# Performance work log

Hardware: AMD Instinct MI355X
Metric: run time of the kernel (lower is better)

The kernel has to match this reference:

```python
import math
import jax, jax.numpy as jnp
import numpy as np

B, D, COND, H, K, L, BOUND = 262144, 16, 8, 128, 10, 4, 1.0
D2 = math.ceil(D / 2)          # second split (spline-transformed channels) = 8
D1 = D - D2                    # passthrough channels = 8
DOUT = (3 * K + 1) * D2        # subnet output = 248
PMIN = 1e-3                    # BIN_WIDTH_MIN == BIN_HEIGHT_MIN == DELTA_MIN


def setup_inputs() -> dict:
    key = jax.random.key(0)
    ks = jax.random.split(key, 8)
    x = jax.random.normal(ks[0], (B, D), dtype=jnp.float32)
    c = jax.random.normal(ks[1], (B, COND), dtype=jnp.float32)
    din1 = D1 + COND
    W1s = jax.random.normal(ks[2], (L, din1, H), dtype=jnp.float32) * 0.1
    b1s = jnp.zeros((L, H), dtype=jnp.float32)
    Whs = jax.random.normal(ks[3], (L, H, H), dtype=jnp.float32) * 0.1
    bhs = jnp.zeros((L, H), dtype=jnp.float32)
    Wos = jax.random.normal(ks[4], (L, H, DOUT), dtype=jnp.float32) * 0.1
    bos = jnp.zeros((L, DOUT), dtype=jnp.float32)
    rng = np.random.default_rng(0)  # permutation_seed = 0
    perms = jnp.asarray(np.stack([rng.permutation(D) for _ in range(L)]), dtype=jnp.int32)
    return {"x": x, "c": c, "W1s": W1s, "b1s": b1s, "Whs": Whs, "bhs": bhs,
            "Wos": Wos, "bos": bos, "perms": perms}


def _softmax_with_min(t, m):
    return m + (1.0 - m * t.shape[-1]) * jax.nn.softmax(t, axis=-1)


def _unpack_theta(theta):
    # theta: [B, D2, 3K+1]
    bw_u, bh_u, ks_u = theta[..., :K], theta[..., K:2 * K], theta[..., 2 * K:]
    bin_w = 2.0 * BOUND * _softmax_with_min(bw_u, PMIN)
    bin_h = 2.0 * BOUND * _softmax_with_min(bh_u, PMIN)
    slopes = PMIN + (1.0 - PMIN) * jax.nn.softplus(ks_u) / math.log(2.0)
    pad = ((0, 0), (0, 0), (1, 0))
    x_knots = jnp.pad(jnp.cumsum(bin_w, axis=-1), pad) - BOUND
    y_knots = jnp.pad(jnp.cumsum(bin_h, axis=-1), pad) - BOUND
    return x_knots, y_knots, bin_w, bin_h, slopes


def _spline_fwd(x2, x_knots, y_knots, bin_w, bin_h, slopes):
    # x2: [B, D2]; knots: [B, D2, K+1]; widths/heights: [B, D2, K]; slopes: [B, D2, K+1]
    bin_idx = jnp.sum(x_knots < x2[..., None], axis=-1) - 1  # searchsorted(left) - 1
    in_bounds = (bin_idx >= 0) & (bin_idx < K)
    ci = jnp.clip(bin_idx, 0, K - 1)
    g = lambda t, i: jnp.take_along_axis(t, i[..., None], axis=-1)[..., 0]
    x1, y1 = g(x_knots, ci), g(y_knots, ci)
    xw, yw = g(bin_w, ci), g(bin_h, ci)
    d1, d2 = g(slopes, ci), g(slopes, ci + 1)
    # safe x so rational-quadratic never produces nan for masked-out lanes
    xs = jnp.where(in_bounds, x2, x1 + 0.5 * xw)
    s = yw / xw
    eta = (xs - x1) / xw
    rev_eta = 1.0 - eta
    err = eta * rev_eta
    y_denom = s + (d1 + d2 - 2.0 * s) * err
    y_rq = y1 + yw * (s * eta ** 2 + d1 * err) / y_denom
    jac_num = s ** 2 * (d2 * eta ** 2 + 2.0 * s * err + d1 * rev_eta ** 2)
    log_jac = jnp.log(jac_num) - 2.0 * jnp.log(y_denom)
    # out-of-bounds: linear extrapolation through the outermost knots
    xl, xr = x_knots[..., 0], x_knots[..., -1]
    yb, yt = y_knots[..., 0], y_knots[..., -1]
    y_lin = (yt - yb) / (xr - xl) * (x2 - xl) + yb
    yx = jnp.where(in_bounds, y_rq, y_lin)
    log_jac = jnp.where(in_bounds, log_jac, 0.0)
    return yx, jnp.sum(log_jac, axis=-1)


def _flow_forward(x, c, W1s, b1s, Whs, bhs, Wos, bos, perms):
    log_jac_det = jnp.zeros((x.shape[0],), dtype=x.dtype)
    for i in range(L):
        x1, x2 = x[:, :D1], x[:, D1:]
        h = jax.nn.relu(jnp.concatenate([x1, c], axis=1) @ W1s[i] + b1s[i])
        h = jax.nn.relu(h @ Whs[i] + bhs[i])
        theta = (h @ Wos[i] + bos[i]).reshape(-1, D2, 3 * K + 1)
        x_knots, y_knots, bin_w, bin_h, slopes = _unpack_theta(theta)
        y2, ljd = _spline_fwd(x2, x_knots, y_knots, bin_w, bin_h, slopes)
        log_jac_det = log_jac_det + ljd
        x_out = jnp.concatenate([x1, y2], axis=1)
        x = jnp.take(x_out, perms[i], axis=1)  # x @ channel_perm.T
    return x, log_jac_det


def reference(x, c, W1s, b1s, Whs, bhs, Wos, bos, perms):
    return _flow_forward(x, c, W1s, b1s, Whs, bhs, Wos, bos, perms)
```

## Files before the change

kernel.cpp:

```cpp
#include <hip/hip_runtime.h>

#define B_N   262144
#define PMIN_F 0.001f
#define LOG2E 1.44269504088896340736f
#define LN2   0.69314718055994530942f

typedef _Float16 half4v __attribute__((ext_vector_type(4)));
typedef _Float16 half8  __attribute__((ext_vector_type(8)));
typedef float    floatx4 __attribute__((ext_vector_type(4)));

__device__ __forceinline__ float fexp2(float x) { return __builtin_amdgcn_exp2f(x); }
__device__ __forceinline__ float flog2(float x) { return __builtin_amdgcn_logf(x); }
__device__ __forceinline__ float frcp (float x) { return __builtin_amdgcn_rcpf(x); }

#define SB() __builtin_amdgcn_sched_barrier(0)

__global__ __launch_bounds__(64) void prep_kernel(
    const float* __restrict__ W1s, const float* __restrict__ b1s,
    const float* __restrict__ Whs, const float* __restrict__ Wos,
    _Float16* __restrict__ ws)
{
    const int bid   = blockIdx.x;
    const int layer = bid / 104;
    const int r     = bid % 104;
    const int lane  = threadIdx.x;
    const int kg    = lane >> 4;
    const int c     = lane & 15;

    half8 v;
    if (r < 8) {
        const int nt = r, n = nt * 16 + c;
        const float* W1 = W1s + layer * 16 * 128;
        const float* b1 = b1s + layer * 128;
        #pragma unroll
        for (int j = 0; j < 8; ++j) {
            const int k = kg * 8 + j;
            v[j] = (k < 16) ? (_Float16)W1[k * 128 + n]
                 : (k == 16) ? (_Float16)b1[n] : (_Float16)0.f;
        }
    } else if (r < 40) {
        const int f = r - 8, nt = f >> 2, ks = f & 3, n = nt * 16 + c;
        const float* Wh = Whs + layer * 128 * 128;
        #pragma unroll
        for (int j = 0; j < 8; ++j) {
            const int k = ks * 32 + kg * 8 + j;
            v[j] = (_Float16)Wh[k * 128 + n];
        }
    } else {
        const int f = r - 40, nt = f >> 2, ks = f & 3, n = nt * 16 + c;
        const int dd = n >> 5, cc = n & 31;
        const float* Wo = Wos + layer * 128 * 248;
        #pragma unroll
        for (int j = 0; j < 8; ++j) {
            const int k = ks * 32 + kg * 8 + j;
            v[j] = (cc < 31) ? (_Float16)Wo[k * 248 + dd * 31 + cc] : (_Float16)0.f;
        }
    }
    *(half8*)(ws + (size_t)bid * 512 + lane * 8) = v;
}

__device__ __forceinline__ void spline_eval(const float* __restrict__ Rf, const int base,
                                            const float x2, float& yout, float& ljout)
{
    const float4 v0 = *(const float4*)&Rf[base];
    const float4 v1 = *(const float4*)&Rf[base + 4];
    const float4 v2 = *(const float4*)&Rf[base + 8];
    const float4 v3 = *(const float4*)&Rf[base + 12];
    const float4 v4 = *(const float4*)&Rf[base + 16];

    float tw[10] = {v0.x, v0.y, v0.z, v0.w, v1.x, v1.y, v1.z, v1.w, v2.x, v2.y};
    float m1 = tw[0];
    #pragma unroll
    for (int i = 1; i < 10; ++i) m1 = fmaxf(m1, tw[i]);
    float se = 0.f;
    #pragma unroll
    for (int i = 0; i < 10; ++i) { tw[i] = fexp2((tw[i] - m1) * LOG2E); se += tw[i]; }
    const float inv198 = 1.98f * frcp(se);

    int cnt = 0;
    {
        float run = -1.f;
        cnt += (run < x2) ? 1 : 0;
        #pragma unroll
        for (int i = 0; i < 10; ++i) {
            run = run + fmaf(tw[i], inv198, 0.002f);
            cnt += (run < x2) ? 1 : 0;
        }
    }
    const int bidx = cnt - 1;
    const bool inb = (bidx >= 0) && (bidx < 10);
    const int ci = bidx < 0 ? 0 : (bidx > 9 ? 9 : bidx);

    float xlo = -1.f, xhi = 0.f, rx;
    {
        float run = -1.f;
        #pragma unroll
        for (int i = 0; i < 10; ++i) {
            const bool pick = (i == ci);
            xlo = pick ? run : xlo;
            run = run + fmaf(tw[i], inv198, 0.002f);
            xhi = pick ? run : xhi;
        }
        rx = run;
    }

    float hh[10] = {v2.z, v2.w, v3.x, v3.y, v3.z, v3.w, v4.x, v4.y, v4.z, v4.w};
    float hm = hh[0];
    #pragma unroll
    for (int i = 1; i < 10; ++i) hm = fmaxf(hm, hh[i]);
    float seh = 0.f;
    #pragma unroll
    for (int i = 0; i < 10; ++i) { hh[i] = fexp2((hh[i] - hm) * LOG2E); seh += hh[i]; }
    const float invh = 1.98f * frcp(seh);
    float ylo = -1.f, yhi = 0.f, ry;
    {
        float run = -1.f;
        #pragma unroll
        for (int i = 0; i < 10; ++i) {
            const bool pick = (i == ci);
            ylo = pick ? run : ylo;
            run = run + fmaf(hh[i], invh, 0.002f);
            yhi = pick ? run : yhi;
        }
        ry = run;
    }

    const float xw = xhi - xlo, yw = yhi - ylo;

    const float u1 = Rf[base + 20 + ci];
    const float u2 = Rf[base + 21 + ci];
    const float t1 = u1 * LOG2E;
    const float t2s = u2 * LOG2E;
    const float dd1 = PMIN_F + 0.999f * ((t1  > 15.f) ? t1  : flog2(1.f + fexp2(t1)));
    const float dd2 = PMIN_F + 0.999f * ((t2s > 15.f) ? t2s : flog2(1.f + fexp2(t2s)));

    const float xs  = inb ? x2 : (xlo + 0.5f * xw);
    const float rxw = frcp(xw);
    const float s   = yw * rxw;
    const float eta = (xs - xlo) * rxw;
    const float rev = 1.f - eta;
    const float er  = eta * rev;
    const float dn  = s + (dd1 + dd2 - 2.f * s) * er;
    const float yrq = ylo + yw * (s * eta * eta + dd1 * er) * frcp(dn);
    const float jn  = s * s * (dd2 * eta * eta + 2.f * s * er + dd1 * rev * rev);
    const float ljx = LN2 * (flog2(jn) - 2.f * flog2(dn));
    const float ylin = (ry + 1.f) * frcp(rx + 1.f) * (x2 + 1.f) - 1.f;

    yout  = inb ? yrq : ylin;
    ljout = inb ? ljx : 0.f;
}

__global__ __launch_bounds__(64, 3) void flow_mfma(
    const float* __restrict__ x_in,
    const float* __restrict__ c_in,
    const float* __restrict__ bhs,
    const float* __restrict__ bos,
    const int*   __restrict__ perms,
    const _Float16* __restrict__ wsW,
    float* __restrict__ out)
{
    __shared__ __align__(16) float    xls[2][256];
    __shared__ __align__(16) _Float16 R[2][2176];

    const int lane = threadIdx.x;
    const int q    = lane >> 4;
    const int m    = lane & 15;
    const long long row0 = (long long)blockIdx.x * 32;

    {
        const float4* xp = (const float4*)(x_in + row0 * 16);
        *(float4*)&xls[0][lane * 4] = xp[lane];
        *(float4*)&xls[1][lane * 4] = xp[lane + 64];
    }

    half8 a1c[2];
    #pragma unroll
    for (int t2 = 0; t2 < 2; ++t2) {
        #pragma unroll
        for (int j = 0; j < 8; ++j) a1c[t2][j] = (_Float16)0.f;
        if (q == 1) {
            const float4* cp = (const float4*)(c_in + (row0 + t2 * 16 + m) * 8);
            const float4 c0 = cp[0], c1 = cp[1];
            a1c[t2][0] = (_Float16)c0.x; a1c[t2][1] = (_Float16)c0.y;
            a1c[t2][2] = (_Float16)c0.z; a1c[t2][3] = (_Float16)c0.w;
            a1c[t2][4] = (_Float16)c1.x; a1c[t2][5] = (_Float16)c1.y;
            a1c[t2][6] = (_Float16)c1.z; a1c[t2][7] = (_Float16)c1.w;
        } else if (q == 2) {
            a1c[t2][0] = (_Float16)1.f;
        }
    }

    const int sp_t2  = lane >> 5;
    const int sp_row = (lane & 31) >> 1;
    const int sp_dl  = lane & 1;

    float ljacc = 0.f;

    for (int l = 0; l < 4; ++l) {
        const _Float16* wsl = wsW + (size_t)l * 104 * 512;
        const float* bh = bhs + l * 128;
        const float* bo = bos + l * 248;

        half8 bf1[8];
        #pragma unroll
        for (int i = 0; i < 8; ++i)
            bf1[i] = *(const half8*)(wsl + i * 512 + lane * 8);
        SB();

        half8 a1[2];
        #pragma unroll
        for (int t2 = 0; t2 < 2; ++t2) {
            a1[t2] = a1c[t2];
            if (q == 0) {
                const float4 lo = *(const float4*)&xls[t2][m * 16];
                const float4 hi = *(const float4*)&xls[t2][m * 16 + 4];
                a1[t2][0] = (_Float16)lo.x; a1[t2][1] = (_Float16)lo.y;
                a1[t2][2] = (_Float16)lo.z; a1[t2][3] = (_Float16)lo.w;
                a1[t2][4] = (_Float16)hi.x; a1[t2][5] = (_Float16)hi.y;
                a1[t2][6] = (_Float16)hi.z; a1[t2][7] = (_Float16)hi.w;
            }
        }
        #pragma unroll
        for (int g = 0; g < 2; ++g) {
            const floatx4 z = {0.f, 0.f, 0.f, 0.f};
            floatx4 acc0[4], acc1[4];
            #pragma unroll
            for (int nt = 0; nt < 4; ++nt) {
                acc0[nt] = __builtin_amdgcn_mfma_f32_16x16x32_f16(a1[0], bf1[g * 4 + nt], z, 0, 0, 0);
                acc1[nt] = __builtin_amdgcn_mfma_f32_16x16x32_f16(a1[1], bf1[g * 4 + nt], z, 0, 0, 0);
            }
            #pragma unroll
            for (int nt = 0; nt < 4; ++nt)
                #pragma unroll
                for (int reg = 0; reg < 4; ++reg) {
                    R[0][(q * 4 + reg) * 132 + (g * 4 + nt) * 16 + m] = (_Float16)fmaxf(acc0[nt][reg], 0.f);
                    R[1][(q * 4 + reg) * 132 + (g * 4 + nt) * 16 + m] = (_Float16)fmaxf(acc1[nt][reg], 0.f);
                }
        }

        half8 bf2a[16];
        #pragma unroll
        for (int i = 0; i < 16; ++i)
            bf2a[i] = *(const half8*)(wsl + (8 + i) * 512 + lane * 8);
        SB();

        half8 a2[2][4];
        #pragma unroll
        for (int t2 = 0; t2 < 2; ++t2)
            #pragma unroll
            for (int ks = 0; ks < 4; ++ks) {
                const half4v lo = *(const half4v*)&R[t2][m * 132 + ks * 32 + q * 8];
                const half4v hi = *(const half4v*)&R[t2][m * 132 + ks * 32 + q * 8 + 4];
                a2[t2][ks] = __builtin_shufflevector(lo, hi, 0, 1, 2, 3, 4, 5, 6, 7);
            }

        floatx4 accA0[4], accA1[4];
        #pragma unroll
        for (int nt = 0; nt < 4; ++nt) {
            const float bb = bh[nt * 16 + m];
            accA0[nt][0] = bb; accA0[nt][1] = bb; accA0[nt][2] = bb; accA0[nt][3] = bb;
            accA1[nt] = accA0[nt];
        }
        #pragma unroll
        for (int ks = 0; ks < 4; ++ks)
            #pragma unroll
            for (int nt = 0; nt < 4; ++nt) {
                accA0[nt] = __builtin_amdgcn_mfma_f32_16x16x32_f16(a2[0][ks], bf2a[nt * 4 + ks], accA0[nt], 0, 0, 0);
                accA1[nt] = __builtin_amdgcn_mfma_f32_16x16x32_f16(a2[1][ks], bf2a[nt * 4 + ks], accA1[nt], 0, 0, 0);
            }

        half8 bf2b[16];
        #pragma unroll
        for (int i = 0; i < 16; ++i)
            bf2b[i] = *(const half8*)(wsl + (24 + i) * 512 + lane * 8);
        SB();

        #pragma unroll
        for (int nt = 0; nt < 4; ++nt)
            #pragma unroll
            for (int reg = 0; reg < 4; ++reg) {
                R[0][(q * 4 + reg) * 132 + nt * 16 + m] = (_Float16)fmaxf(accA0[nt][reg], 0.f);
                R[1][(q * 4 + reg) * 132 + nt * 16 + m] = (_Float16)fmaxf(accA1[nt][reg], 0.f);
            }

        floatx4 accB0[4], accB1[4];
        #pragma unroll
        for (int nt = 0; nt < 4; ++nt) {
            const float bb = bh[(4 + nt) * 16 + m];
            accB0[nt][0] = bb; accB0[nt][1] = bb; accB0[nt][2] = bb; accB0[nt][3] = bb;
            accB1[nt] = accB0[nt];
        }
        #pragma unroll
        for (int ks = 0; ks < 4; ++ks)
            #pragma unroll
            for (int nt = 0; nt < 4; ++nt) {
                accB0[nt] = __builtin_amdgcn_mfma_f32_16x16x32_f16(a2[0][ks], bf2b[nt * 4 + ks], accB0[nt], 0, 0, 0);
                accB1[nt] = __builtin_amdgcn_mfma_f32_16x16x32_f16(a2[1][ks], bf2b[nt * 4 + ks], accB1[nt], 0, 0, 0);
            }
        #pragma unroll
        for (int nt = 0; nt < 4; ++nt)
            #pragma unroll
            for (int reg = 0; reg < 4; ++reg) {
                R[0][(q * 4 + reg) * 132 + (4 + nt) * 16 + m] = (_Float16)fmaxf(accB0[nt][reg], 0.f);
                R[1][(q * 4 + reg) * 132 + (4 + nt) * 16 + m] = (_Float16)fmaxf(accB1[nt][reg], 0.f);
            }

        half8 bf3[16];
        #pragma unroll
        for (int i = 0; i < 16; ++i)
            bf3[i] = *(const half8*)(wsl + (40 + i) * 512 + lane * 8);
        SB();

        half8 a3[2][4];
        #pragma unroll
        for (int t2 = 0; t2 < 2; ++t2)
            #pragma unroll
            for (int ks = 0; ks < 4; ++ks) {
                const half4v lo = *(const half4v*)&R[t2][m * 132 + ks * 32 + q * 8];
                const half4v hi = *(const half4v*)&R[t2][m * 132 + ks * 32 + q * 8 + 4];
                a3[t2][ks] = __builtin_shufflevector(lo, hi, 0, 1, 2, 3, 4, 5, 6, 7);
            }
        __syncthreads();

        float* Rf0 = (float*)&R[0][0];
        float* Rf1 = (float*)&R[1][0];

        #pragma unroll
        for (int qd = 0; qd < 4; ++qd) {
            floatx4 acc0[4], acc1[4];
            {
                #pragma unroll
                for (int j = 0; j < 4; ++j) {
                    const int n = qd * 64 + j * 16 + m;
                    const int cc = n & 31;
                    const float bb = (cc < 31) ? bo[(n >> 5) * 31 + cc] : 0.f;
                    acc0[j][0] = bb; acc0[j][1] = bb; acc0[j][2] = bb; acc0[j][3] = bb;
                    acc1[j] = acc0[j];
                }
                #pragma unroll
                for (int ks = 0; ks < 4; ++ks)
                    #pragma unroll
                    for (int j = 0; j < 4; ++j) {
                        acc0[j] = __builtin_amdgcn_mfma_f32_16x16x32_f16(a3[0][ks], bf3[j * 4 + ks], acc0[j], 0, 0, 0);
                        acc1[j] = __builtin_amdgcn_mfma_f32_16x16x32_f16(a3[1][ks], bf3[j * 4 + ks], acc1[j], 0, 0, 0);
                    }
            }

            if (qd < 3) {
                #pragma unroll
                for (int i = 0; i < 16; ++i)
                    bf3[i] = *(const half8*)(wsl + (40 + (qd + 1) * 16 + i) * 512 + lane * 8);
                SB();
            }

            #pragma unroll
            for (int j = 0; j < 4; ++j) {
                const int off = (j >> 1) * 32 + (j & 1) * 16 + m;
                #pragma unroll
                for (int reg = 0; reg < 4; ++reg) {
                    Rf0[(q * 4 + reg) * 68 + off] = acc0[j][reg];
                    Rf1[(q * 4 + reg) * 68 + off] = acc1[j][reg];
                }
            }

            {
                const int d    = qd * 2 + sp_dl;
                const int base = sp_row * 68 + sp_dl * 32;
                const float* Rf = sp_t2 ? Rf1 : Rf0;
                const int xi   = sp_row * 16 + 8 + d;

                float yv, lj;
                spline_eval(Rf, base, xls[sp_t2][xi], yv, lj);
                xls[sp_t2][xi] = yv;
                ljacc += lj;
            }
        }

        {
            const int4 pv = ((const int4*)(perms + l * 16))[lane & 3];
            const int mm = lane >> 2;
            const float a0 = xls[0][mm * 16 + pv.x];
            const float a1v = xls[0][mm * 16 + pv.y];
            const float a2v = xls[0][mm * 16 + pv.z];
            const float a3v = xls[0][mm * 16 + pv.w];
            const float b0 = xls[1][mm * 16 + pv.x];
            const float b1v = xls[1][mm * 16 + pv.y];
            const float b2 = xls[1][mm * 16 + pv.z];
            const float b3 = xls[1][mm * 16 + pv.w];
            *(float4*)&xls[0][lane * 4] = make_float4(a0, a1v, a2v, a3v);
            *(float4*)&xls[1][lane * 4] = make_float4(b0, b1v, b2, b3);
        }
        __syncthreads();
    }

    #pragma unroll
    for (int t2 = 0; t2 < 2; ++t2) {
        const float4 vo = *(const float4*)&xls[t2][lane * 4];
        ((float4*)(out + (row0 + t2 * 16) * 16))[lane] = vo;
    }
    {
        const float ljs = ljacc + __shfl_xor(ljacc, 1);
        if ((lane & 1) == 0)
            out[(size_t)B_N * 16 + row0 + sp_t2 * 16 + sp_row] = ljs;
    }
}

extern "C" void kernel_launch(void* const* d_in, const int* in_sizes, int n_in,
                              void* d_out, int out_size, void* d_ws, size_t ws_size,
                              hipStream_t stream) {
    const float* x     = (const float*)d_in[0];
    const float* c     = (const float*)d_in[1];
    const float* W1s   = (const float*)d_in[2];
    const float* b1s   = (const float*)d_in[3];
    const float* Whs   = (const float*)d_in[4];
    const float* bhs   = (const float*)d_in[5];
    const float* Wos   = (const float*)d_in[6];
    const float* bos   = (const float*)d_in[7];
    const int*   perms = (const int*)d_in[8];
    float* out = (float*)d_out;
    _Float16* ws = (_Float16*)d_ws;

    prep_kernel<<<dim3(416), dim3(64), 0, stream>>>(W1s, b1s, Whs, Wos, ws);
    flow_mfma<<<dim3(B_N / 32), dim3(64), 0, stream>>>(
        x, c, bhs, bos, perms, ws, out);
}
```

Before: 273.4 us.

## Prefetch next-layer weights and split output-weight loads to overlap spline work

Moves the first-layer weight fragment load out of the loop and prefetches the next layer's fragment before the permutation step. The output-layer weight buffer is split into two halves, and the second half is reloaded after the spline evaluation so global loads overlap spline math. The occupancy hint also changes from launch_bounds min-blocks to an explicit waves_per_eu(3,3). This is meant to hide weight-load latency behind compute, at the cost of possibly higher register pressure at a fixed occupancy target.

Result: slower. 303.1 us (+10.8%).

```diff
diff --git a/kernel.cpp b/kernel.cpp
--- a/kernel.cpp
+++ b/kernel.cpp
@@ -150,7 +150,8 @@
     ljout = inb ? ljx : 0.f;
 }
 
-__global__ __launch_bounds__(64, 3) void flow_mfma(
+__global__ __attribute__((amdgpu_waves_per_eu(3, 3))) __launch_bounds__(64)
+void flow_mfma(
     const float* __restrict__ x_in,
     const float* __restrict__ c_in,
     const float* __restrict__ bhs,
@@ -196,16 +197,16 @@
 
     float ljacc = 0.f;
 
+    half8 bf1[8];
+    #pragma unroll
+    for (int i = 0; i < 8; ++i)
+        bf1[i] = *(const half8*)(wsW + i * 512 + lane * 8);
+    SB();
+
     for (int l = 0; l < 4; ++l) {
         const _Float16* wsl = wsW + (size_t)l * 104 * 512;
         const float* bh = bhs + l * 128;
         const float* bo = bos + l * 248;
-
-        half8 bf1[8];
-        #pragma unroll
-        for (int i = 0; i < 8; ++i)
-            bf1[i] = *(const half8*)(wsl + i * 512 + lane * 8);
-        SB();
 
         half8 a1[2];
         #pragma unroll
@@ -305,10 +306,13 @@
                 R[1][(q * 4 + reg) * 132 + (4 + nt) * 16 + m] = (_Float16)fmaxf(accB1[nt][reg], 0.f);
             }
 
-        half8 bf3[16];
-        #pragma unroll
-        for (int i = 0; i < 16; ++i)
-            bf3[i] = *(const half8*)(wsl + (40 + i) * 512 + lane * 8);
+        half8 bf3a[8], bf3b[8];
+        #pragma unroll
+        for (int i = 0; i < 8; ++i)
+            bf3a[i] = *(const half8*)(wsl + (40 + i) * 512 + lane * 8);
+        #pragma unroll
+        for (int i = 0; i < 8; ++i)
+            bf3b[i] = *(const half8*)(wsl + (48 + i) * 512 + lane * 8);
         SB();
 
         half8 a3[2][4];
@@ -341,15 +345,16 @@
                 for (int ks = 0; ks < 4; ++ks)
                     #pragma unroll
                     for (int j = 0; j < 4; ++j) {
-                        acc0[j] = __builtin_amdgcn_mfma_f32_16x16x32_f16(a3[0][ks], bf3[j * 4 + ks], acc0[j], 0, 0, 0);
-                        acc1[j] = __builtin_amdgcn_mfma_f32_16x16x32_f16(a3[1][ks], bf3[j * 4 + ks], acc1[j], 0, 0, 0);
+                        const half8 b = (j < 2) ? bf3a[j * 4 + ks] : bf3b[(j - 2) * 4 + ks];
+                        acc0[j] = __builtin_amdgcn_mfma_f32_16x16x32_f16(a3[0][ks], b, acc0[j], 0, 0, 0);
+                        acc1[j] = __builtin_amdgcn_mfma_f32_16x16x32_f16(a3[1][ks], b, acc1[j], 0, 0, 0);
                     }
             }
 
             if (qd < 3) {
                 #pragma unroll
-                for (int i = 0; i < 16; ++i)
-                    bf3[i] = *(const half8*)(wsl + (40 + (qd + 1) * 16 + i) * 512 + lane * 8);
+                for (int i = 0; i < 8; ++i)
+                    bf3a[i] = *(const half8*)(wsl + (40 + (qd + 1) * 16 + i) * 512 + lane * 8);
                 SB();
             }
 
@@ -374,6 +379,21 @@
                 xls[sp_t2][xi] = yv;
                 ljacc += lj;
             }
+
+            if (qd < 3) {
+                #pragma unroll
+                for (int i = 0; i < 8; ++i)
+                    bf3b[i] = *(const half8*)(wsl + (48 + (qd + 1) * 16 + i) * 512 + lane * 8);
+                SB();
+            }
+        }
+
+        if (l < 3) {
+            const _Float16* wsn = wsW + (size_t)(l + 1) * 104 * 512;
+            #pragma unroll
+            for (int i = 0; i < 8; ++i)
+                bf1[i] = *(const half8*)(wsn + i * 512 + lane * 8);
+            SB();
         }
 
         {
```
